# Kernel optimization log

Hardware: AMD Instinct MI355X
Metric: run time of the kernel (lower is better)

The kernel has to match this reference:

```python
import jax, jax.numpy as jnp
import numpy as np

B, L, D = 32, 2048, 1024


def setup_inputs() -> dict:
    key = jax.random.key(0)
    ks = jax.random.split(key, 6)
    x = jax.random.normal(ks[0], (B, L, D), dtype=jnp.float32)
    # lambda_log = log(U(0.7, 0.9)) per original init
    lam0 = jax.random.uniform(ks[1], (D,), minval=0.7, maxval=0.9, dtype=jnp.float32)
    lambda_log = jnp.log(lam0)
    gamma = jnp.ones((D,), dtype=jnp.float32)
    # nn.Linear weights [out, in], xavier-ish scale
    scale = 1.0 / np.sqrt(D)
    W_in = jax.random.normal(ks[2], (D, D), dtype=jnp.float32) * scale
    b_in = jnp.zeros((D,), dtype=jnp.float32)
    W_out = jax.random.normal(ks[3], (D, D), dtype=jnp.float32) * scale
    b_out = jnp.zeros((D,), dtype=jnp.float32)
    return {"x": x, "lambda_log": lambda_log, "gamma": gamma,
            "W_in": W_in, "b_in": b_in, "W_out": W_out, "b_out": b_out}


def reference(x, lambda_log, gamma, W_in, b_in, W_out, b_out):
    # u = input_proj(x)  (nn.Linear: x @ W.T + b)
    u = jnp.einsum('bld,ed->ble', x, W_in) + b_in
    lam = jnp.exp(lambda_log)            # [D]
    gu = gamma * u                        # [B, L, D]
    # diagonal linear recurrence h_t = lam * h_{t-1} + gu_t, scanned over time
    def step(h, gu_t):
        h = lam * h + gu_t
        return h, h
    _, hs = jax.lax.scan(step, jnp.zeros((x.shape[0], x.shape[2]), x.dtype),
                         jnp.swapaxes(gu, 0, 1))   # hs: [L, B, D]
    y = jnp.swapaxes(hs, 0, 1)            # [B, L, D]
    # dropout is identity in eval mode
    out = jnp.einsum('bld,ed->ble', y, W_out) + b_out + x
    return out
```

## Files before the change

### kernel.cpp

```cpp
#include <hip/hip_runtime.h>
#include <hip/hip_bf16.h>
#include <stdint.h>

#define Bdim 32
#define Ldim 2048
#define Ddim 1024
#define Mdim (Bdim*Ldim)

typedef __attribute__((ext_vector_type(8))) short short8;
typedef __attribute__((ext_vector_type(8))) __bf16 bf16x8;
typedef __attribute__((ext_vector_type(4))) float f32x4;

__device__ __forceinline__ unsigned short f2bf(float v) {
    unsigned u = __float_as_uint(v);
    u += 0x7FFFu + ((u >> 16) & 1u);
    return (unsigned short)(u >> 16);
}
__device__ __forceinline__ float bf2f(unsigned short h) {
    return __uint_as_float(((unsigned)h) << 16);
}
__device__ __forceinline__ void split2(float v, unsigned short& hi, unsigned short& lo) {
    hi = f2bf(v);
    float rem = v - bf2f(hi);
    lo = f2bf(rem);
}

__global__ __launch_bounds__(256) void k_split(const float* __restrict__ in,
        unsigned short* __restrict__ hi, unsigned short* __restrict__ lo, int n4) {
    int i = blockIdx.x*blockDim.x + threadIdx.x;
    int stride = gridDim.x*blockDim.x;
    for (; i < n4; i += stride) {
        float4 v = ((const float4*)in)[i];
        ushort4 h, l;
        split2(v.x, h.x, l.x);
        split2(v.y, h.y, l.y);
        split2(v.z, h.z, l.z);
        split2(v.w, h.w, l.w);
        ((ushort4*)hi)[i] = h;
        ((ushort4*)lo)[i] = l;
    }
}

__global__ __launch_bounds__(256, 2) void k_gemm(
        const unsigned short* __restrict__ Ahi, const unsigned short* __restrict__ Alo,
        const unsigned short* __restrict__ Whi, const unsigned short* __restrict__ Wlo,
        const float* __restrict__ bias, const float* __restrict__ gamma,
        const float* __restrict__ resid, float* __restrict__ out, int mode) {
    __shared__ unsigned short lds[32768];
    const int tid  = threadIdx.x;
    const int w    = tid >> 6;
    const int lane = tid & 63;
    const int m0 = blockIdx.y * 128;
    const int n0 = blockIdx.x * 128;
    const int wr = w >> 1, wc = w & 1;

    const unsigned short* src = (w==0)?Ahi:((w==1)?Alo:((w==2)?Whi:Wlo));
    const int rowbase = (w < 2) ? m0 : n0;
    const int lr = lane >> 3;
    const int lc = (lane & 7) * 8;

    f32x4 acc[4][4];
    #pragma unroll
    for (int i=0;i<4;++i)
      #pragma unroll
      for (int j=0;j<4;++j) acc[i][j] = (f32x4){0.f,0.f,0.f,0.f};

    const int row_a = lane & 15;
    const int ksel  = (lane >> 4) * 8;

    for (int kt = 0; kt < Ddim/64; ++kt) {
        const int k0 = kt*64;
        #pragma unroll
        for (int i = 0; i < 16; ++i) {
            const unsigned short* gp = src + (size_t)(rowbase + i*8 + lr)*Ddim + (k0 + lc);
            unsigned short* lp = &lds[w*8192 + i*512];
            __builtin_amdgcn_global_load_lds(
                (const __attribute__((address_space(1))) void*)gp,
                (__attribute__((address_space(3))) void*)lp, 16, 0, 0);
        }
        __syncthreads();
        #pragma unroll
        for (int kk = 0; kk < 64; kk += 32) {
            short8 ah[4], al[4], bh[4], bl[4];
            #pragma unroll
            for (int f=0; f<4; ++f) {
                const int ar = wr*64 + f*16 + row_a;
                const int br = wc*64 + f*16 + row_a;
                ah[f] = *(const short8*)&lds[0*8192 + ar*64 + kk + ksel];
                al[f] = *(const short8*)&lds[1*8192 + ar*64 + kk + ksel];
                bh[f] = *(const short8*)&lds[2*8192 + br*64 + kk + ksel];
                bl[f] = *(const short8*)&lds[3*8192 + br*64 + kk + ksel];
            }
            #pragma unroll
            for (int mi=0; mi<4; ++mi) {
              #pragma unroll
              for (int ni=0; ni<4; ++ni) {
                acc[mi][ni] = __builtin_amdgcn_mfma_f32_16x16x32_bf16(
                    __builtin_bit_cast(bf16x8, ah[mi]), __builtin_bit_cast(bf16x8, bh[ni]),
                    acc[mi][ni], 0, 0, 0);
                acc[mi][ni] = __builtin_amdgcn_mfma_f32_16x16x32_bf16(
                    __builtin_bit_cast(bf16x8, ah[mi]), __builtin_bit_cast(bf16x8, bl[ni]),
                    acc[mi][ni], 0, 0, 0);
                acc[mi][ni] = __builtin_amdgcn_mfma_f32_16x16x32_bf16(
                    __builtin_bit_cast(bf16x8, al[mi]), __builtin_bit_cast(bf16x8, bh[ni]),
                    acc[mi][ni], 0, 0, 0);
              }
            }
        }
        __syncthreads();
    }

    const int crow0 = (lane >> 4) * 4;
    const int ccol  = lane & 15;
    #pragma unroll
    for (int mi=0; mi<4; ++mi) {
      #pragma unroll
      for (int ni=0; ni<4; ++ni) {
        const int col = n0 + wc*64 + ni*16 + ccol;
        const float bv = bias[col];
        const float gv = (mode == 0) ? gamma[col] : 1.f;
        #pragma unroll
        for (int r=0; r<4; ++r) {
          const int row = m0 + wr*64 + mi*16 + crow0 + r;
          const size_t idx = (size_t)row*Ddim + col;
          const float v = acc[mi][ni][r];
          if (mode == 0) out[idx] = gv * (v + bv);
          else           out[idx] = v + bv + resid[idx];
        }
      }
    }
}

__global__ __launch_bounds__(64) void k_scan(const float* __restrict__ gu,
        const float* __restrict__ lambda_log,
        unsigned short* __restrict__ yhi, unsigned short* __restrict__ ylo) {
    const int d = blockIdx.x*64 + threadIdx.x;
    const int b = blockIdx.y;
    const float lam = expf(lambda_log[d]);
    const size_t base = (size_t)b*Ldim*Ddim + d;
    float h = 0.f;
    for (int t0 = 0; t0 < Ldim; t0 += 16) {
        float g[16];
        #pragma unroll
        for (int j=0;j<16;++j) g[j] = gu[base + (size_t)(t0+j)*Ddim];
        #pragma unroll
        for (int j=0;j<16;++j) {
            h = fmaf(lam, h, g[j]);
            unsigned short hi, lo; split2(h, hi, lo);
            yhi[base + (size_t)(t0+j)*Ddim] = hi;
            ylo[base + (size_t)(t0+j)*Ddim] = lo;
        }
    }
}

extern "C" void kernel_launch(void* const* d_in, const int* in_sizes, int n_in,
                              void* d_out, int out_size, void* d_ws, size_t ws_size,
                              hipStream_t stream) {
    const float* x          = (const float*)d_in[0];
    const float* lambda_log = (const float*)d_in[1];
    const float* gamma      = (const float*)d_in[2];
    const float* W_in       = (const float*)d_in[3];
    const float* b_in       = (const float*)d_in[4];
    const float* W_out      = (const float*)d_in[5];
    const float* b_out      = (const float*)d_in[6];
    float* out = (float*)d_out;

    unsigned short* xhi  = (unsigned short*)d_ws;
    unsigned short* xlo  = xhi  + (size_t)Mdim*Ddim;
    unsigned short* wihi = xlo  + (size_t)Mdim*Ddim;
    unsigned short* wilo = wihi + (size_t)Ddim*Ddim;
    unsigned short* wohi = wilo + (size_t)Ddim*Ddim;
    unsigned short* wolo = wohi + (size_t)Ddim*Ddim;
    float*          gu   = (float*)(wolo + (size_t)Ddim*Ddim);

    k_split<<<2048, 256, 0, stream>>>(x,     xhi,  xlo,  Mdim*Ddim/4);
    k_split<<<128,  256, 0, stream>>>(W_in,  wihi, wilo, Ddim*Ddim/4);
    k_split<<<128,  256, 0, stream>>>(W_out, wohi, wolo, Ddim*Ddim/4);

    k_gemm<<<dim3(Ddim/128, Mdim/128), 256, 0, stream>>>(
        xhi, xlo, wihi, wilo, b_in, gamma, nullptr, gu, 0);

    k_scan<<<dim3(Ddim/64, Bdim), 64, 0, stream>>>(gu, lambda_log, xhi, xlo);

    k_gemm<<<dim3(Ddim/128, Mdim/128), 256, 0, stream>>>(
        xhi, xlo, wohi, wolo, b_out, nullptr, x, out, 1);
}
```

Measured before the change: 1.716 ms.

## Parallelize scan over time segments, swizzle GEMM LDS, and remap tile order

The serial time scan is split into three passes: per-segment local sums, a carry propagation across 8 segments using lam^SEG, and a final pass that rescans each segment from its carry. This exposes more parallelism than the original 32x16 small-block grid, at the cost of reading gu twice. The GEMM also gets an XOR swizzle on LDS columns to cut bank conflicts, and a block-index remap so that blocks sharing the same A rows run close together for better L2 reuse. hseg and carry reuse the W_in split buffers, which are no longer needed after the first GEMM.

```diff
diff --git a/kernel.cpp b/kernel.cpp
--- a/kernel.cpp
+++ b/kernel.cpp
@@ -6,6 +6,8 @@
 #define Ldim 2048
 #define Ddim 1024
 #define Mdim (Bdim*Ldim)
+#define NSEG 8
+#define SEG  (Ldim/NSEG)
 
 typedef __attribute__((ext_vector_type(8))) short short8;
 typedef __attribute__((ext_vector_type(8))) __bf16 bf16x8;
@@ -50,14 +52,16 @@
     const int tid  = threadIdx.x;
     const int w    = tid >> 6;
     const int lane = tid & 63;
-    const int m0 = blockIdx.y * 128;
-    const int n0 = blockIdx.x * 128;
+    const int m_t = (blockIdx.y & ~7u) | blockIdx.x;
+    const int n_t = blockIdx.y & 7u;
+    const int m0 = m_t * 128;
+    const int n0 = n_t * 128;
     const int wr = w >> 1, wc = w & 1;
 
     const unsigned short* src = (w==0)?Ahi:((w==1)?Alo:((w==2)?Whi:Wlo));
     const int rowbase = (w < 2) ? m0 : n0;
     const int lr = lane >> 3;
-    const int lc = (lane & 7) * 8;
+    const int lc = ((lane & 7) ^ lr) * 8;
 
     f32x4 acc[4][4];
     #pragma unroll
@@ -66,7 +70,8 @@
       for (int j=0;j<4;++j) acc[i][j] = (f32x4){0.f,0.f,0.f,0.f};
 
     const int row_a = lane & 15;
-    const int ksel  = (lane >> 4) * 8;
+    const int kgrp  = lane >> 4;
+    const int l7    = lane & 7;
 
     for (int kt = 0; kt < Ddim/64; ++kt) {
         const int k0 = kt*64;
@@ -81,15 +86,16 @@
         __syncthreads();
         #pragma unroll
         for (int kk = 0; kk < 64; kk += 32) {
+            const int coff = (((kk >> 3) + kgrp) ^ l7) * 8;
             short8 ah[4], al[4], bh[4], bl[4];
             #pragma unroll
             for (int f=0; f<4; ++f) {
                 const int ar = wr*64 + f*16 + row_a;
                 const int br = wc*64 + f*16 + row_a;
-                ah[f] = *(const short8*)&lds[0*8192 + ar*64 + kk + ksel];
-                al[f] = *(const short8*)&lds[1*8192 + ar*64 + kk + ksel];
-                bh[f] = *(const short8*)&lds[2*8192 + br*64 + kk + ksel];
-                bl[f] = *(const short8*)&lds[3*8192 + br*64 + kk + ksel];
+                ah[f] = *(const short8*)&lds[0*8192 + ar*64 + coff];
+                al[f] = *(const short8*)&lds[1*8192 + ar*64 + coff];
+                bh[f] = *(const short8*)&lds[2*8192 + br*64 + coff];
+                bl[f] = *(const short8*)&lds[3*8192 + br*64 + coff];
             }
             #pragma unroll
             for (int mi=0; mi<4; ++mi) {
@@ -131,24 +137,58 @@
     }
 }
 
-__global__ __launch_bounds__(64) void k_scan(const float* __restrict__ gu,
-        const float* __restrict__ lambda_log,
+__global__ __launch_bounds__(256) void k_scan1(const float* __restrict__ gu,
+        const float* __restrict__ lambda_log, float* __restrict__ hseg) {
+    const int d = blockIdx.x*256 + threadIdx.x;
+    const int b = blockIdx.y;
+    const int s = blockIdx.z;
+    const float lam = expf(lambda_log[d]);
+    const size_t base = (size_t)b*Ldim*Ddim + (size_t)s*SEG*Ddim + d;
+    float h = 0.f;
+    for (int t0 = 0; t0 < SEG; t0 += 8) {
+        float g[8];
+        #pragma unroll
+        for (int j=0;j<8;++j) g[j] = gu[base + (size_t)(t0+j)*Ddim];
+        #pragma unroll
+        for (int j=0;j<8;++j) h = fmaf(lam, h, g[j]);
+    }
+    hseg[((size_t)s*Bdim + b)*Ddim + d] = h;
+}
+
+__global__ __launch_bounds__(256) void k_scan2(const float* __restrict__ hseg,
+        const float* __restrict__ lambda_log, float* __restrict__ carry) {
+    const int ch = blockIdx.x*256 + threadIdx.x;
+    const int b = ch >> 10;
+    const int d = ch & 1023;
+    const float lamS = expf(lambda_log[d] * (float)SEG);
+    float c = 0.f;
+    #pragma unroll
+    for (int s = 0; s < NSEG; ++s) {
+        carry[((size_t)s*Bdim + b)*Ddim + d] = c;
+        c = fmaf(lamS, c, hseg[((size_t)s*Bdim + b)*Ddim + d]);
+    }
+}
+
+__global__ __launch_bounds__(256) void k_scan3(const float* __restrict__ gu,
+        const float* __restrict__ lambda_log, const float* __restrict__ carry,
         unsigned short* __restrict__ yhi, unsigned short* __restrict__ ylo) {
-    const int d = blockIdx.x*64 + threadIdx.x;
+    const int d = blockIdx.x*256 + threadIdx.x;
     const int b = blockIdx.y;
+    const int s = blockIdx.z;
     const float lam = expf(lambda_log[d]);
-    const size_t base = (size_t)b*Ldim*Ddim + d;
-    float h = 0.f;
-    for (int t0 = 0; t0 < Ldim; t0 += 16) {
-        float g[16];
-        #pragma unroll
-        for (int j=0;j<16;++j) g[j] = gu[base + (size_t)(t0+j)*Ddim];
-        #pragma unroll
-        for (int j=0;j<16;++j) {
+    const size_t base = (size_t)b*Ldim*Ddim + (size_t)s*SEG*Ddim + d;
+    float h = carry[((size_t)s*Bdim + b)*Ddim + d];
+    for (int t0 = 0; t0 < SEG; t0 += 8) {
+        float g[8];
+        #pragma unroll
+        for (int j=0;j<8;++j) g[j] = gu[base + (size_t)(t0+j)*Ddim];
+        #pragma unroll
+        for (int j=0;j<8;++j) {
             h = fmaf(lam, h, g[j]);
             unsigned short hi, lo; split2(h, hi, lo);
-            yhi[base + (size_t)(t0+j)*Ddim] = hi;
-            ylo[base + (size_t)(t0+j)*Ddim] = lo;
+            const size_t idx = base + (size_t)(t0+j)*Ddim;
+            yhi[idx] = hi;
+            ylo[idx] = lo;
         }
     }
 }
@@ -172,16 +212,20 @@
     unsigned short* wohi = wilo + (size_t)Ddim*Ddim;
     unsigned short* wolo = wohi + (size_t)Ddim*Ddim;
     float*          gu   = (float*)(wolo + (size_t)Ddim*Ddim);
+    float* hseg  = (float*)wihi;
+    float* carry = (float*)wilo;
 
     k_split<<<2048, 256, 0, stream>>>(x,     xhi,  xlo,  Mdim*Ddim/4);
     k_split<<<128,  256, 0, stream>>>(W_in,  wihi, wilo, Ddim*Ddim/4);
     k_split<<<128,  256, 0, stream>>>(W_out, wohi, wolo, Ddim*Ddim/4);
 
-    k_gemm<<<dim3(Ddim/128, Mdim/128), 256, 0, stream>>>(
+    k_gemm<<<dim3(8, Mdim/128), 256, 0, stream>>>(
         xhi, xlo, wihi, wilo, b_in, gamma, nullptr, gu, 0);
 
-    k_scan<<<dim3(Ddim/64, Bdim), 64, 0, stream>>>(gu, lambda_log, xhi, xlo);
-
-    k_gemm<<<dim3(Ddim/128, Mdim/128), 256, 0, stream>>>(
+    k_scan1<<<dim3(Ddim/256, Bdim, NSEG), 256, 0, stream>>>(gu, lambda_log, hseg);
+    k_scan2<<<(Bdim*Ddim)/256, 256, 0, stream>>>(hseg, lambda_log, carry);
+    k_scan3<<<dim3(Ddim/256, Bdim, NSEG), 256, 0, stream>>>(gu, lambda_log, carry, xhi, xlo);
+
+    k_gemm<<<dim3(8, Mdim/128), 256, 0, stream>>>(
         xhi, xlo, wohi, wolo, b_out, nullptr, x, out, 1);
 }
```

Measured after the change: 1.610 ms. -6.2%, faster.
